# Kernel tuning notes

Measured on AMD Instinct MI355X. Metric: run time of the kernel, lower is better.

The kernel has to match this reference:

```python
import jax, jax.numpy as jnp
import numpy as np

H = 16  # num_attention_heads


def setup_inputs() -> dict:
    key = jax.random.key(0)
    ks = jax.random.split(key, 4)
    B, S, D = 2, 2048, 1024
    hidden_states = jax.random.normal(ks[0], (B, S, D), dtype=jnp.float32)
    attention_mask = jnp.zeros((B, 1, 1, S), dtype=jnp.float32)
    scale = 1.0 / np.sqrt(D)
    Wq = jax.random.normal(ks[1], (D, D), dtype=jnp.float32) * scale
    Wk = jax.random.normal(ks[2], (D, D), dtype=jnp.float32) * scale
    Wv = jax.random.normal(ks[3], (D, D), dtype=jnp.float32) * scale
    bq = jnp.zeros((D,), dtype=jnp.float32)
    bk = jnp.zeros((D,), dtype=jnp.float32)
    bv = jnp.zeros((D,), dtype=jnp.float32)
    return {"hidden_states": hidden_states, "attention_mask": attention_mask,
            "Wq": Wq, "bq": bq, "Wk": Wk, "bk": bk, "Wv": Wv, "bv": bv}


def reference(hidden_states, attention_mask, Wq, bq, Wk, bk, Wv, bv):
    B, S, D = hidden_states.shape
    Dh = D // H

    def proj(W, b):
        # torch Linear: x @ W.T + b ; reshape to [B, H, S, Dh]
        y = jnp.einsum('bsd,ed->bse', hidden_states, W) + b
        return y.reshape(B, S, H, Dh).transpose(0, 2, 1, 3)

    q = proj(Wq, bq)
    k = proj(Wk, bk)
    v = proj(Wv, bv)

    scores = jnp.einsum('bhqd,bhkd->bhqk', q, k) / jnp.sqrt(jnp.float32(Dh))
    scores = scores + attention_mask  # additive mask broadcast [B,1,1,S]
    probs = jax.nn.softmax(scores, axis=-1)  # [B,H,Sq,Sk]
    out_attention_scores = probs.sum(axis=-2).sum(axis=-2)  # [B, Sk]
    # dropout prob = 0 (eval) -> identity
    context = jnp.einsum('bhqk,bhkd->bhqd', probs, v)
    context = context.transpose(0, 2, 1, 3).reshape(B, S, D)
    return context, out_attention_scores
```

## Files before the change

kernel.cpp:

```cpp
#include <hip/hip_runtime.h>
#include <hip/hip_bf16.h>
#include <stdint.h>

typedef unsigned short u16;
typedef __attribute__((ext_vector_type(8))) unsigned short u16x8;
typedef __attribute__((ext_vector_type(4))) unsigned short u16x4;
typedef __attribute__((ext_vector_type(8))) __bf16 bf16x8;
typedef __attribute__((ext_vector_type(4))) float f32x4;
typedef __attribute__((ext_vector_type(16))) float f32x16;

#define LOG2E 1.44269504088896340736f

#if defined(__has_builtin)
#if __has_builtin(__builtin_amdgcn_exp2f)
#define EXP2(x) __builtin_amdgcn_exp2f(x)
#endif
#endif
#ifndef EXP2
#define EXP2(x) exp2f(x)
#endif

__device__ __forceinline__ f32x4 mfma16(u16x8 a, u16x8 b, f32x4 c) {
  return __builtin_amdgcn_mfma_f32_16x16x32_bf16(
      __builtin_bit_cast(bf16x8, a), __builtin_bit_cast(bf16x8, b), c, 0, 0, 0);
}

__device__ __forceinline__ f32x16 mfma32(u16x8 a, u16x8 b, f32x16 c) {
  return __builtin_amdgcn_mfma_f32_32x32x16_bf16(
      __builtin_bit_cast(bf16x8, a), __builtin_bit_cast(bf16x8, b), c, 0, 0, 0);
}

__device__ __forceinline__ u16 f2bf(float f) {
  unsigned u = __builtin_bit_cast(unsigned, f);
  return (u16)((u + 0x7fffu + ((u >> 16) & 1u)) >> 16);
}

__device__ __forceinline__ unsigned cvtpk(float a, float b) {
  unsigned r;
  asm volatile("v_cvt_pk_bf16_f32 %0, %1, %2" : "=v"(r) : "v"(a), "v"(b));
  return r;
}

__device__ __forceinline__ void pswap(unsigned& a, unsigned& b) {
  asm volatile("v_permlane32_swap_b32 %0, %1" : "+v"(a), "+v"(b));
}

__device__ __forceinline__ void gload_lds16(const void* g, void* l) {
  __builtin_amdgcn_global_load_lds(
      (__attribute__((address_space(1))) void*)const_cast<void*>(g),
      (__attribute__((address_space(3))) void*)l, 16, 0, 0);
}

template<int N> __device__ __forceinline__ void vmwait() {
  __builtin_amdgcn_sched_barrier(0);
  asm volatile("s_waitcnt vmcnt(%0)" :: "n"(N) : "memory");
  __builtin_amdgcn_sched_barrier(0);
}

#define SWZ(row, colbyte) ((((row) * 128) + (colbyte)) ^ (((row) & 7) << 4))

__global__ void cast_all(const float* __restrict__ X,
                         const float* __restrict__ s0, const float* __restrict__ s1,
                         const float* __restrict__ s2,
                         u16* __restrict__ Xb, u16* __restrict__ Wcat) {
  const int bid = blockIdx.x;
  const float* src;
  u16* dst;
  int i;
  if (bid < 4096) {
    src = X; dst = Xb;
    i = bid * 256 + threadIdx.x;
  } else {
    const int wb = bid - 4096;
    const int seg = wb >> 10;
    src = (seg == 0) ? s0 : ((seg == 1) ? s1 : s2);
    dst = Wcat + (size_t)seg * 1048576;
    i = (wb & 1023) * 256 + threadIdx.x;
  }
  f32x4 v = ((const f32x4*)src)[i];
  u16x4 o;
  o[0] = f2bf(v[0]); o[1] = f2bf(v[1]); o[2] = f2bf(v[2]); o[3] = f2bf(v[3]);
  ((u16x4*)dst)[i] = o;
}

__global__ __launch_bounds__(256) void gemm_qkv(
    const u16* __restrict__ A, const u16* __restrict__ Bm,
    const float* __restrict__ bq, const float* __restrict__ bk, const float* __restrict__ bv,
    u16* __restrict__ Qb, u16* __restrict__ Kb, u16* __restrict__ VTb) {
  __shared__ __align__(16) u16 Asm[3][4096];
  __shared__ __align__(16) u16 Bsm[3][4096];
  const int tid = threadIdx.x;
  const int wave = tid >> 6, lane = tid & 63;
  const int lq = lane & 15, lg = lane >> 4;
  const int wr = wave >> 1, wc = wave & 1;
  const int lin = blockIdx.y * 24 + blockIdx.x;
  const int wg = (lin & 7) * 96 + (lin >> 3);
  const int m0 = (wg / 24) * 128, n0 = (wg % 24) * 128;

  f32x4 zero = {0.f, 0.f, 0.f, 0.f};
  f32x4 acc[4][4];
#pragma unroll
  for (int mi = 0; mi < 4; ++mi)
#pragma unroll
    for (int ni = 0; ni < 4; ++ni) acc[mi][ni] = zero;

  int rA0, k16A0, rA1, k16A1;
  {
    const int cc0 = wave * 128 + lane;
    const int ln0 = cc0 >> 3, sp0 = (cc0 & 7) ^ (ln0 & 7);
    rA0 = ln0 * 2 + (sp0 >> 2); k16A0 = sp0 & 3;
    const int cc1 = cc0 + 64;
    const int ln1 = cc1 >> 3, sp1 = (cc1 & 7) ^ (ln1 & 7);
    rA1 = ln1 * 2 + (sp1 >> 2); k16A1 = sp1 & 3;
  }

  auto stage = [&](int kt, int buf) {
    const int kk = kt * 32;
    gload_lds16(A + (size_t)(m0 + rA0) * 1024 + kk + k16A0 * 8,
                (char*)&Asm[buf][0] + (wave * 2 + 0) * 1024);
    gload_lds16(A + (size_t)(m0 + rA1) * 1024 + kk + k16A1 * 8,
                (char*)&Asm[buf][0] + (wave * 2 + 1) * 1024);
    gload_lds16(Bm + (size_t)(n0 + rA0) * 1024 + kk + k16A0 * 8,
                (char*)&Bsm[buf][0] + (wave * 2 + 0) * 1024);
    gload_lds16(Bm + (size_t)(n0 + rA1) * 1024 + kk + k16A1 * 8,
                (char*)&Bsm[buf][0] + (wave * 2 + 1) * 1024);
  };

  stage(0, 0);
  stage(1, 1);
  for (int kt = 0; kt < 32; ++kt) {
    if (kt < 31) vmwait<4>(); else vmwait<0>();
    __builtin_amdgcn_s_barrier();
    if (kt + 2 < 32) stage(kt + 2, (kt + 2) % 3);
    const int cur = kt % 3;

    __builtin_amdgcn_s_setprio(1);
    u16x8 af[4], bfr[4];
#pragma unroll
    for (int mi = 0; mi < 4; ++mi) {
      const int rA = wr * 64 + mi * 16 + lq;
      const int lnA = rA >> 1;
      const int spA = ((rA & 1) << 2) | lg;
      af[mi] = *(const u16x8*)((const char*)&Asm[cur][0] +
                               lnA * 128 + ((spA ^ (lnA & 7)) << 4));
    }
#pragma unroll
    for (int ni = 0; ni < 4; ++ni) {
      const int rB = wc * 64 + ni * 16 + lq;
      const int lnB = rB >> 1;
      const int spB = ((rB & 1) << 2) | lg;
      bfr[ni] = *(const u16x8*)((const char*)&Bsm[cur][0] +
                                lnB * 128 + ((spB ^ (lnB & 7)) << 4));
    }
#pragma unroll
    for (int mi = 0; mi < 4; ++mi)
#pragma unroll
      for (int ni = 0; ni < 4; ++ni)
        acc[mi][ni] = mfma16(af[mi], bfr[ni], acc[mi][ni]);
    __builtin_amdgcn_s_setprio(0);
  }

  const int which = n0 >> 10;
  const float* bias = (which == 0) ? bq : ((which == 1) ? bk : bv);
  const float scl = (which == 0) ? (0.125f * LOG2E) : 1.0f;
#pragma unroll
  for (int mi = 0; mi < 4; ++mi) {
    const int m = m0 + wr * 64 + mi * 16 + lg * 4;
    const int bb = m >> 11;
    const int s = m & 2047;
#pragma unroll
    for (int ni = 0; ni < 4; ++ni) {
      const int n = n0 + wc * 64 + ni * 16 + lq;
      const int d = n & 1023;
      const int h = d >> 6, dh = d & 63;
      const float bi = bias[d];
#pragma unroll
      for (int r = 0; r < 4; ++r) {
        float v = (acc[mi][ni][r] + bi) * scl;
        if (which == 2)
          VTb[(((size_t)bb * 16 + h) * 64 + dh) * 2048 + (size_t)(s + r)] = f2bf(v);
        else {
          u16* dst = (which == 0) ? Qb : Kb;
          dst[(((size_t)bb * 16 + h) * 2048 + (size_t)(s + r)) * 64 + dh] = f2bf(v);
        }
      }
    }
  }
}

__global__ __launch_bounds__(512) void attn_pair(
    const u16* __restrict__ Qb, const u16* __restrict__ Kb, const u16* __restrict__ VTb,
    const float* __restrict__ maskg, float* __restrict__ out_ctx, float* __restrict__ winv) {
  __shared__ __align__(16) char smem[65536];

  const int tid = threadIdx.x;
  const int w = tid >> 6, lane = tid & 63;
  const int l31 = lane & 31, h = lane >> 5;
  const int hf = w >> 2, p = w & 3;
  const int bid = (blockIdx.x & 7) * 64 + (blockIdx.x >> 3);
  const int qt = bid & 15, bh = bid >> 4;
  const int b = bh >> 4, hh = bh & 15;
  const int qw = qt * 128 + p * 32;

  const u16* qp = Qb + ((size_t)bh * 2048 + qw + l31) * 64 + h * 8;
  u16x8 qa[4];
#pragma unroll
  for (int dq = 0; dq < 4; ++dq) qa[dq] = *(const u16x8*)(qp + dq * 16);

  const char* KbaseG = (const char*)(Kb + (size_t)bh * 2048 * 64);
  const char* VTbaseG = (const char*)(VTb + (size_t)bh * 64 * 2048);
  const float* mbase = maskg + b * 2048;

  const int t8 = tid & 255;
  const int srowK = t8 >> 3;
  const int scolK = ((t8 & 7) * 16) ^ ((srowK & 7) << 4);
  const int lineV = t8 >> 3;
  const int spV = (t8 & 7) ^ (lineV & 7);
  const int dhV = lineV * 2 + (spV >> 2);
  const int kbV = (spV & 3) * 16;

  auto stage = [&](int kt, int buf) {
    char* kd = smem + hf * 16384 + buf * 4096 + (w & 3) * 1024;
    gload_lds16(KbaseG + (size_t)(kt * 32 + srowK) * 128 + scolK, kd);
    char* vd = smem + 32768 + hf * 16384 + buf * 4096 + (w & 3) * 1024;
    gload_lds16(VTbaseG + (size_t)dhV * 4096 + (size_t)kt * 64 + kbV, vd);
  };

  f32x16 accpv[2];
#pragma unroll
  for (int db = 0; db < 2; ++db)
#pragma unroll
    for (int r = 0; r < 16; ++r) accpv[db][r] = 0.f;
  float l_l = 0.f;

  const int kt0 = hf * 32;
  stage(kt0, 0);
  stage(kt0 + 1, 1);
  stage(kt0 + 2, 2);
  for (int j = 0; j < 32; ++j) {
    const int kt = kt0 + j;
    if (j < 30) vmwait<4>(); else if (j == 30) vmwait<2>(); else vmwait<0>();
    __builtin_amdgcn_s_barrier();
    const char* Kt = smem + hf * 16384 + (j & 3) * 4096;
    const char* Vt = smem + 32768 + hf * 16384 + (j & 3) * 4096;

    __builtin_amdgcn_s_setprio(1);
    f32x16 s;
#pragma unroll
    for (int r = 0; r < 16; ++r) s[r] = 0.f;
#pragma unroll
    for (int dq = 0; dq < 4; ++dq) {
      const u16x8 ka = *(const u16x8*)(Kt + SWZ(l31, dq * 32 + h * 16));
      s = mfma32(ka, qa[dq], s);
    }
    float pv[16];
#pragma unroll
    for (int g = 0; g < 4; ++g) {
      const f32x4 mv = *(const f32x4*)(mbase + kt * 32 + g * 8 + h * 4);
#pragma unroll
      for (int j2 = 0; j2 < 4; ++j2)
        pv[g * 4 + j2] = EXP2(fmaf(mv[j2], LOG2E, s[g * 4 + j2]));
    }
    l_l += ((pv[0] + pv[1]) + (pv[2] + pv[3])) + ((pv[4] + pv[5]) + (pv[6] + pv[7])) +
           ((pv[8] + pv[9]) + (pv[10] + pv[11])) + ((pv[12] + pv[13]) + (pv[14] + pv[15]));
    unsigned a01 = cvtpk(pv[0], pv[1]), a23 = cvtpk(pv[2], pv[3]);
    unsigned a45 = cvtpk(pv[4], pv[5]), a67 = cvtpk(pv[6], pv[7]);
    unsigned b01 = cvtpk(pv[8], pv[9]), b23 = cvtpk(pv[10], pv[11]);
    unsigned b45 = cvtpk(pv[12], pv[13]), b67 = cvtpk(pv[14], pv[15]);
    pswap(a01, a45); pswap(a23, a67);
    pswap(b01, b45); pswap(b23, b67);
    uint4 f1 = {a01, a23, a45, a67};
    uint4 f2 = {b01, b23, b45, b67};
    u16x8 pf[2] = {__builtin_bit_cast(u16x8, f1), __builtin_bit_cast(u16x8, f2)};
#pragma unroll
    for (int ks2 = 0; ks2 < 2; ++ks2) {
#pragma unroll
      for (int db = 0; db < 2; ++db) {
        const int rowV = db * 32 + l31;
        const int lnV = rowV >> 1;
        const int sV = ((rowV & 1) << 2) | (ks2 << 1) | h;
        const u16x8 vt = *(const u16x8*)(Vt + lnV * 128 + ((sV ^ (lnV & 7)) << 4));
        accpv[db] = mfma32(pf[ks2], vt, accpv[db]);
      }
    }
    __builtin_amdgcn_s_setprio(0);
    __builtin_amdgcn_sched_barrier(0);
    if (j + 3 < 32) stage(kt0 + j + 3, (j + 3) & 3);
  }

  l_l += __shfl_xor(l_l, 32);

  __syncthreads();
  float* pairctx = (float*)smem;
  float* pairl = (float*)(smem + 32768);
  if (hf == 1) {
#pragma unroll
    for (int db = 0; db < 2; ++db)
#pragma unroll
      for (int r = 0; r < 16; ++r) {
        const int q = (r & 3) + (r >> 2) * 8 + h * 4;
        pairctx[p * 2048 + q * 64 + db * 32 + l31] = accpv[db][r];
      }
    if (h == 0) pairl[p * 32 + l31] = l_l;
  }
  __syncthreads();
  if (hf == 0) {
    const float lt = l_l + pairl[p * 32 + l31];
    const float il = 1.0f / lt;
    if (h == 0) winv[bh * 2048 + qw + l31] = il;
#pragma unroll
    for (int r = 0; r < 16; ++r) {
      const int q = (r & 3) + (r >> 2) * 8 + h * 4;
      const float ilr = __shfl(il, q);
      const size_t row = (size_t)(b * 2048 + qw + q) * 1024 + hh * 64;
      out_ctx[row + l31] = (accpv[0][r] + pairctx[p * 2048 + q * 64 + l31]) * ilr;
      out_ctx[row + 32 + l31] = (accpv[1][r] + pairctx[p * 2048 + q * 64 + 32 + l31]) * ilr;
    }
  }
}

__global__ __launch_bounds__(256) void colsum_kernel(
    const u16* __restrict__ Qb, const u16* __restrict__ Kb,
    const float* __restrict__ maskg, const float* __restrict__ winv,
    float* __restrict__ out_cs) {
  __shared__ __align__(16) u16 Ql[3][4096];

  const int tid = threadIdx.x;
  const int w = tid >> 6, lane = tid & 63;
  const int lq = lane & 15, lg = lane >> 4;
  const int bid = (blockIdx.x & 7) * 128 + (blockIdx.x >> 3);
  const int ktile = bid & 7, qq = (bid >> 3) & 3, bh = bid >> 5;
  const int b = bh >> 4;
  const int kbase = ktile * 256 + w * 64;
  const int q0t = qq * 8;

  const u16* kp = Kb + ((size_t)bh * 2048 + kbase + lq) * 64 + lg * 8;
  u16x8 kf[4][2];
  float mvl[4];
#pragma unroll
  for (int g = 0; g < 4; ++g) {
    kf[g][0] = *(const u16x8*)(kp + (size_t)g * 16 * 64);
    kf[g][1] = *(const u16x8*)(kp + (size_t)g * 16 * 64 + 32);
    mvl[g] = maskg[b * 2048 + kbase + g * 16 + lq] * LOG2E;
  }
  const float* wbase = winv + bh * 2048;
  const char* Qbase = (const char*)(Qb + (size_t)bh * 2048 * 64);

  const int r0 = tid >> 3;
  const int scol = ((tid & 7) * 16) ^ ((r0 & 7) << 4);
  auto stageQ = [&](int qt, int buf) {
    const char* src = Qbase + (size_t)(qt * 64) * 128;
    char* d = (char*)&Ql[buf][0] + w * 1024;
    gload_lds16(src + (size_t)r0 * 128 + scol, d);
    gload_lds16(src + (size_t)(r0 + 32) * 128 + scol, d + 4096);
  };

  float c0 = 0.f, c1 = 0.f, c2 = 0.f, c3 = 0.f;
  stageQ(q0t, 0);
  stageQ(q0t + 1, 1);
  for (int j = 0; j < 8; ++j) {
    const int qt = q0t + j;
    if (j < 7) vmwait<2>(); else vmwait<0>();
    __builtin_amdgcn_s_barrier();
    const char* Qt = (const char*)&Ql[j % 3][0];
    __builtin_amdgcn_s_setprio(1);
#pragma unroll
    for (int chunk = 0; chunk < 4; ++chunk) {
      const u16x8 qf0 = *(const u16x8*)(Qt + SWZ(chunk * 16 + lq, lg * 16));
      const u16x8 qf1 = *(const u16x8*)(Qt + SWZ(chunk * 16 + lq, 64 + lg * 16));
      const f32x4 wv = *(const f32x4*)(wbase + qt * 64 + chunk * 16 + lg * 4);
      f32x4 z = {0.f, 0.f, 0.f, 0.f};
      f32x4 s0 = mfma16(qf0, kf[0][0], z); s0 = mfma16(qf1, kf[0][1], s0);
      f32x4 s1 = mfma16(qf0, kf[1][0], z); s1 = mfma16(qf1, kf[1][1], s1);
      f32x4 s2 = mfma16(qf0, kf[2][0], z); s2 = mfma16(qf1, kf[2][1], s2);
      f32x4 s3 = mfma16(qf0, kf[3][0], z); s3 = mfma16(qf1, kf[3][1], s3);
#pragma unroll
      for (int r = 0; r < 4; ++r) {
        c0 += EXP2(s0[r] + mvl[0]) * wv[r];
        c1 += EXP2(s1[r] + mvl[1]) * wv[r];
        c2 += EXP2(s2[r] + mvl[2]) * wv[r];
        c3 += EXP2(s3[r] + mvl[3]) * wv[r];
      }
    }
    __builtin_amdgcn_s_setprio(0);
    __builtin_amdgcn_sched_barrier(0);
    if (j + 2 < 8) stageQ(q0t + j + 2, (j + 2) % 3);
  }
  c0 += __shfl_xor(c0, 16); c0 += __shfl_xor(c0, 32);
  c1 += __shfl_xor(c1, 16); c1 += __shfl_xor(c1, 32);
  c2 += __shfl_xor(c2, 16); c2 += __shfl_xor(c2, 32);
  c3 += __shfl_xor(c3, 16); c3 += __shfl_xor(c3, 32);
  if (lg == 0) {
    atomicAdd(&out_cs[b * 2048 + kbase + lq], c0);
    atomicAdd(&out_cs[b * 2048 + kbase + 16 + lq], c1);
    atomicAdd(&out_cs[b * 2048 + kbase + 32 + lq], c2);
    atomicAdd(&out_cs[b * 2048 + kbase + 48 + lq], c3);
  }
}

extern "C" void kernel_launch(void* const* d_in, const int* in_sizes, int n_in,
                              void* d_out, int out_size, void* d_ws, size_t ws_size,
                              hipStream_t stream) {
  (void)in_sizes; (void)n_in; (void)out_size; (void)ws_size;
  const float* X    = (const float*)d_in[0];
  const float* mask = (const float*)d_in[1];
  const float* Wq   = (const float*)d_in[2];
  const float* bq   = (const float*)d_in[3];
  const float* Wk   = (const float*)d_in[4];
  const float* bk   = (const float*)d_in[5];
  const float* Wv   = (const float*)d_in[6];
  const float* bv   = (const float*)d_in[7];
  float* out = (float*)d_out;

  char* ws = (char*)d_ws;
  u16* Xb   = (u16*)(ws);
  u16* Wcat = (u16*)(ws + 8388608);
  u16* Qb   = (u16*)(ws + 14680064);
  u16* Kb   = (u16*)(ws + 23068672);
  u16* VTb  = (u16*)(ws + 31457280);
  float* winv = (float*)(ws + 39845888);

  hipMemsetAsync(out + 4194304, 0, 4096 * sizeof(float), stream);

  cast_all<<<7168, 256, 0, stream>>>(X, Wq, Wk, Wv, Xb, Wcat);

  gemm_qkv<<<dim3(24, 32), 256, 0, stream>>>(Xb, Wcat, bq, bk, bv, Qb, Kb, VTb);

  attn_pair<<<512, 512, 0, stream>>>(Qb, Kb, VTb, mask, out, winv);
  colsum_kernel<<<1024, 256, 0, stream>>>(Qb, Kb, mask, winv, out + 4194304);
}
```

Before: 139.7 us.

## Prescale mask, fold it into MFMA accumulator init, stage mask/winv in LDS

The cast kernel now also produces a LOG2E-prescaled copy of the mask and zeroes the column-sum output, which removes the separate memset launch. In attention and colsum the scaled mask becomes the initial MFMA accumulator, so the per-element fma before exp2 goes away. Attention caches the mask row in LDS and drops from four to three K/V stage buffers, cutting LDS use with a shallower prefetch. Colsum caches winv in LDS and uses fmaf for accumulation; the shallower pipeline may expose more load latency.

```diff
diff --git a/kernel.cpp b/kernel.cpp
--- a/kernel.cpp
+++ b/kernel.cpp
@@ -61,9 +61,19 @@
 
 __global__ void cast_all(const float* __restrict__ X,
                          const float* __restrict__ s0, const float* __restrict__ s1,
-                         const float* __restrict__ s2,
-                         u16* __restrict__ Xb, u16* __restrict__ Wcat) {
+                         const float* __restrict__ s2, const float* __restrict__ mask,
+                         u16* __restrict__ Xb, u16* __restrict__ Wcat,
+                         float* __restrict__ maskL, float* __restrict__ out_cs) {
   const int bid = blockIdx.x;
+  if (bid >= 7168) {
+    const int i = (bid - 7168) * 256 + threadIdx.x;
+    f32x4 m = ((const f32x4*)mask)[i];
+    m[0] *= LOG2E; m[1] *= LOG2E; m[2] *= LOG2E; m[3] *= LOG2E;
+    ((f32x4*)maskL)[i] = m;
+    f32x4 z = {0.f, 0.f, 0.f, 0.f};
+    ((f32x4*)out_cs)[i] = z;
+    return;
+  }
   const float* src;
   u16* dst;
   int i;
@@ -190,8 +200,8 @@
 
 __global__ __launch_bounds__(512) void attn_pair(
     const u16* __restrict__ Qb, const u16* __restrict__ Kb, const u16* __restrict__ VTb,
-    const float* __restrict__ maskg, float* __restrict__ out_ctx, float* __restrict__ winv) {
-  __shared__ __align__(16) char smem[65536];
+    const float* __restrict__ maskL, float* __restrict__ out_ctx, float* __restrict__ winv) {
+  __shared__ __align__(16) char smem[57344];
 
   const int tid = threadIdx.x;
   const int w = tid >> 6, lane = tid & 63;
@@ -202,6 +212,12 @@
   const int b = bh >> 4, hh = bh & 15;
   const int qw = qt * 128 + p * 32;
 
+  float* maskLds = (float*)(smem + 49152);
+  {
+    const f32x4 m = ((const f32x4*)(maskL + b * 2048))[tid];
+    *(f32x4*)(maskLds + tid * 4) = m;
+  }
+
   const u16* qp = Qb + ((size_t)bh * 2048 + qw + l31) * 64 + h * 8;
   u16x8 qa[4];
 #pragma unroll
@@ -209,7 +225,6 @@
 
   const char* KbaseG = (const char*)(Kb + (size_t)bh * 2048 * 64);
   const char* VTbaseG = (const char*)(VTb + (size_t)bh * 64 * 2048);
-  const float* mbase = maskg + b * 2048;
 
   const int t8 = tid & 255;
   const int srowK = t8 >> 3;
@@ -220,9 +235,9 @@
   const int kbV = (spV & 3) * 16;
 
   auto stage = [&](int kt, int buf) {
-    char* kd = smem + hf * 16384 + buf * 4096 + (w & 3) * 1024;
+    char* kd = smem + hf * 12288 + buf * 4096 + (w & 3) * 1024;
     gload_lds16(KbaseG + (size_t)(kt * 32 + srowK) * 128 + scolK, kd);
-    char* vd = smem + 32768 + hf * 16384 + buf * 4096 + (w & 3) * 1024;
+    char* vd = smem + 24576 + hf * 12288 + buf * 4096 + (w & 3) * 1024;
     gload_lds16(VTbaseG + (size_t)dhV * 4096 + (size_t)kt * 64 + kbV, vd);
   };
 
@@ -233,21 +248,28 @@
     for (int r = 0; r < 16; ++r) accpv[db][r] = 0.f;
   float l_l = 0.f;
 
+  __syncthreads();
   const int kt0 = hf * 32;
   stage(kt0, 0);
   stage(kt0 + 1, 1);
-  stage(kt0 + 2, 2);
   for (int j = 0; j < 32; ++j) {
     const int kt = kt0 + j;
-    if (j < 30) vmwait<4>(); else if (j == 30) vmwait<2>(); else vmwait<0>();
+    if (j < 31) vmwait<2>(); else vmwait<0>();
     __builtin_amdgcn_s_barrier();
-    const char* Kt = smem + hf * 16384 + (j & 3) * 4096;
-    const char* Vt = smem + 32768 + hf * 16384 + (j & 3) * 4096;
+    const char* Kt = smem + hf * 12288 + (j % 3) * 4096;
+    const char* Vt = smem + 24576 + hf * 12288 + (j % 3) * 4096;
 
     __builtin_amdgcn_s_setprio(1);
     f32x16 s;
-#pragma unroll
-    for (int r = 0; r < 16; ++r) s[r] = 0.f;
+    {
+      const float* mrow = maskLds + kt * 32 + h * 4;
+#pragma unroll
+      for (int g = 0; g < 4; ++g) {
+        const f32x4 mv = *(const f32x4*)(mrow + g * 8);
+        s[g * 4 + 0] = mv[0]; s[g * 4 + 1] = mv[1];
+        s[g * 4 + 2] = mv[2]; s[g * 4 + 3] = mv[3];
+      }
+    }
 #pragma unroll
     for (int dq = 0; dq < 4; ++dq) {
       const u16x8 ka = *(const u16x8*)(Kt + SWZ(l31, dq * 32 + h * 16));
@@ -255,12 +277,7 @@
     }
     float pv[16];
 #pragma unroll
-    for (int g = 0; g < 4; ++g) {
-      const f32x4 mv = *(const f32x4*)(mbase + kt * 32 + g * 8 + h * 4);
-#pragma unroll
-      for (int j2 = 0; j2 < 4; ++j2)
-        pv[g * 4 + j2] = EXP2(fmaf(mv[j2], LOG2E, s[g * 4 + j2]));
-    }
+    for (int r = 0; r < 16; ++r) pv[r] = EXP2(s[r]);
     l_l += ((pv[0] + pv[1]) + (pv[2] + pv[3])) + ((pv[4] + pv[5]) + (pv[6] + pv[7])) +
            ((pv[8] + pv[9]) + (pv[10] + pv[11])) + ((pv[12] + pv[13]) + (pv[14] + pv[15]));
     unsigned a01 = cvtpk(pv[0], pv[1]), a23 = cvtpk(pv[2], pv[3]);
@@ -285,7 +302,7 @@
     }
     __builtin_amdgcn_s_setprio(0);
     __builtin_amdgcn_sched_barrier(0);
-    if (j + 3 < 32) stage(kt0 + j + 3, (j + 3) & 3);
+    if (j + 2 < 32) stage(kt0 + j + 2, (j + 2) % 3);
   }
 
   l_l += __shfl_xor(l_l, 32);
@@ -321,9 +338,10 @@
 
 __global__ __launch_bounds__(256) void colsum_kernel(
     const u16* __restrict__ Qb, const u16* __restrict__ Kb,
-    const float* __restrict__ maskg, const float* __restrict__ winv,
+    const float* __restrict__ maskL, const float* __restrict__ winv,
     float* __restrict__ out_cs) {
   __shared__ __align__(16) u16 Ql[3][4096];
+  __shared__ float winvLds[512];
 
   const int tid = threadIdx.x;
   const int w = tid >> 6, lane = tid & 63;
@@ -334,16 +352,21 @@
   const int kbase = ktile * 256 + w * 64;
   const int q0t = qq * 8;
 
+  if (tid < 128) {
+    const f32x4 v = ((const f32x4*)(winv + (size_t)bh * 2048 + q0t * 64))[tid];
+    *(f32x4*)(winvLds + tid * 4) = v;
+  }
+
   const u16* kp = Kb + ((size_t)bh * 2048 + kbase + lq) * 64 + lg * 8;
   u16x8 kf[4][2];
-  float mvl[4];
+  f32x4 zg[4];
 #pragma unroll
   for (int g = 0; g < 4; ++g) {
     kf[g][0] = *(const u16x8*)(kp + (size_t)g * 16 * 64);
     kf[g][1] = *(const u16x8*)(kp + (size_t)g * 16 * 64 + 32);
-    mvl[g] = maskg[b * 2048 + kbase + g * 16 + lq] * LOG2E;
-  }
-  const float* wbase = winv + bh * 2048;
+    const float m = maskL[b * 2048 + kbase + g * 16 + lq];
+    zg[g][0] = m; zg[g][1] = m; zg[g][2] = m; zg[g][3] = m;
+  }
   const char* Qbase = (const char*)(Qb + (size_t)bh * 2048 * 64);
 
   const int r0 = tid >> 3;
@@ -356,10 +379,10 @@
   };
 
   float c0 = 0.f, c1 = 0.f, c2 = 0.f, c3 = 0.f;
+  __syncthreads();
   stageQ(q0t, 0);
   stageQ(q0t + 1, 1);
   for (int j = 0; j < 8; ++j) {
-    const int qt = q0t + j;
     if (j < 7) vmwait<2>(); else vmwait<0>();
     __builtin_amdgcn_s_barrier();
     const char* Qt = (const char*)&Ql[j % 3][0];
@@ -368,18 +391,17 @@
     for (int chunk = 0; chunk < 4; ++chunk) {
       const u16x8 qf0 = *(const u16x8*)(Qt + SWZ(chunk * 16 + lq, lg * 16));
       const u16x8 qf1 = *(const u16x8*)(Qt + SWZ(chunk * 16 + lq, 64 + lg * 16));
-      const f32x4 wv = *(const f32x4*)(wbase + qt * 64 + chunk * 16 + lg * 4);
-      f32x4 z = {0.f, 0.f, 0.f, 0.f};
-      f32x4 s0 = mfma16(qf0, kf[0][0], z); s0 = mfma16(qf1, kf[0][1], s0);
-      f32x4 s1 = mfma16(qf0, kf[1][0], z); s1 = mfma16(qf1, kf[1][1], s1);
-      f32x4 s2 = mfma16(qf0, kf[2][0], z); s2 = mfma16(qf1, kf[2][1], s2);
-      f32x4 s3 = mfma16(qf0, kf[3][0], z); s3 = mfma16(qf1, kf[3][1], s3);
+      const f32x4 wv = *(const f32x4*)(winvLds + j * 64 + chunk * 16 + lg * 4);
+      f32x4 s0 = mfma16(qf0, kf[0][0], zg[0]); s0 = mfma16(qf1, kf[0][1], s0);
+      f32x4 s1 = mfma16(qf0, kf[1][0], zg[1]); s1 = mfma16(qf1, kf[1][1], s1);
+      f32x4 s2 = mfma16(qf0, kf[2][0], zg[2]); s2 = mfma16(qf1, kf[2][1], s2);
+      f32x4 s3 = mfma16(qf0, kf[3][0], zg[3]); s3 = mfma16(qf1, kf[3][1], s3);
 #pragma unroll
       for (int r = 0; r < 4; ++r) {
-        c0 += EXP2(s0[r] + mvl[0]) * wv[r];
-        c1 += EXP2(s1[r] + mvl[1]) * wv[r];
-        c2 += EXP2(s2[r] + mvl[2]) * wv[r];
-        c3 += EXP2(s3[r] + mvl[3]) * wv[r];
+        c0 = fmaf(EXP2(s0[r]), wv[r], c0);
+        c1 = fmaf(EXP2(s1[r]), wv[r], c1);
+        c2 = fmaf(EXP2(s2[r]), wv[r], c2);
+        c3 = fmaf(EXP2(s3[r]), wv[r], c3);
       }
     }
     __builtin_amdgcn_s_setprio(0);
@@ -418,14 +440,14 @@
   u16* Qb   = (u16*)(ws + 14680064);
   u16* Kb   = (u16*)(ws + 23068672);
   u16* VTb  = (u16*)(ws + 31457280);
-  float* winv = (float*)(ws + 39845888);
-
-  hipMemsetAsync(out + 4194304, 0, 4096 * sizeof(float), stream);
-
-  cast_all<<<7168, 256, 0, stream>>>(X, Wq, Wk, Wv, Xb, Wcat);
+  float* winv  = (float*)(ws + 39845888);
+  float* maskL = (float*)(ws + 40108032);
+
+  cast_all<<<7172, 256, 0, stream>>>(X, Wq, Wk, Wv, mask, Xb, Wcat,
+                                     maskL, out + 4194304);
 
   gemm_qkv<<<dim3(24, 32), 256, 0, stream>>>(Xb, Wcat, bq, bk, bv, Qb, Kb, VTb);
 
-  attn_pair<<<512, 512, 0, stream>>>(Qb, Kb, VTb, mask, out, winv);
-  colsum_kernel<<<1024, 256, 0, stream>>>(Qb, Kb, mask, winv, out + 4194304);
-}
+  attn_pair<<<512, 512, 0, stream>>>(Qb, Kb, VTb, maskL, out, winv);
+  colsum_kernel<<<1024, 256, 0, stream>>>(Qb, Kb, maskL, winv, out + 4194304);
+}
```

New measurement: 127.5 us (median of 2 runs). -8.8%, faster.
